# Performance work log

Measured on AMD Instinct MI355X. Metric: run time of the kernel, lower is better.

The kernel has to match this reference:

```python
import jax, jax.numpy as jnp
import numpy as np

LN_EPS = 1e-5


def setup_inputs() -> dict:
    key = jax.random.key(0)
    k1, k2, k3 = jax.random.split(key, 3)
    B, K, S, H, D = 8, 32, 4096, 2048, 1024
    plan_embeddings = jax.random.normal(k1, (B, S, H), dtype=jnp.float32)
    ownership = jax.random.bernoulli(k2, 0.5, (B, K, S))  # bool (B, K, S)
    W = jax.random.normal(k3, (H, D), dtype=jnp.float32) * (1.0 / np.sqrt(H))
    b = jnp.zeros((D,), dtype=jnp.float32)
    gamma = jnp.ones((D,), dtype=jnp.float32)
    beta = jnp.zeros((D,), dtype=jnp.float32)
    return {
        "plan_embeddings": plan_embeddings,
        "ownership": ownership,
        "W": W,
        "b": b,
        "gamma": gamma,
        "beta": beta,
    }


def reference(plan_embeddings, ownership, W, b, gamma, beta):
    # ownership-weighted mean pooling over slots S (same math as the
    # broadcast-multiply + sum in the torch original, expressed as an einsum
    # so no (B,K,S,H) intermediate is materialized)
    own_f = ownership.astype(plan_embeddings.dtype)          # (B, K, S)
    summed = jnp.einsum('bks,bsh->bkh', own_f, plan_embeddings)  # (B, K, H)
    counts = jnp.clip(own_f.sum(axis=-1, keepdims=True), 1.0)   # (B, K, 1)
    pooled = summed / counts                                   # (B, K, H)
    # linear projection
    projected = pooled @ W + b                                 # (B, K, D)
    # LayerNorm over last dim
    mu = projected.mean(axis=-1, keepdims=True)
    var = jnp.mean(jnp.square(projected - mu), axis=-1, keepdims=True)
    normed = (projected - mu) * jax.lax.rsqrt(var + LN_EPS)
    return normed * gamma + beta
```

## Files before the change

### kernel.cpp

```cpp
#include <hip/hip_runtime.h>

typedef unsigned int u32;
typedef unsigned short u16;
typedef __attribute__((ext_vector_type(8))) short short8;
typedef __attribute__((ext_vector_type(4))) float f32x4;
typedef __attribute__((ext_vector_type(16))) float f32x16;

#define BB 8
#define KK 32
#define SS 4096
#define HH 2048
#define DD 1024
#define NSC 16
#define SC_S 256
#define CH (BB * KK * HH)

#define OFF_W16  0ull
#define OFF_WB   (2ull << 20)
#define OFF_PART (6ull << 20)
#define OFF_PQ   (23ull << 20)
#define OFF_PROJ (24ull << 20)

__device__ __forceinline__ u16 f2bf(float x) {
  u32 u = __float_as_uint(x);
  return (u16)((u + 0x7fffu + ((u >> 16) & 1u)) >> 16);
}

__global__ __launch_bounds__(256) void k_prep(const void* __restrict__ own,
                                              u16* __restrict__ w16,
                                              const float* __restrict__ W,
                                              u16* __restrict__ WB) {
  __shared__ float lds[64][65];
  const int t = threadIdx.x;

  if (blockIdx.x < BB * KK) {
    const int bk = blockIdx.x;
    __shared__ int s_mode;
    __shared__ int s_wcnt[4];
    __shared__ float s_inv;

    if (t < 64) {
      u32 w = ((const u32*)own)[t];
      bool wordok = (w <= 1u) || (w == 0x3f800000u);
      unsigned long long m = __ballot(wordok);
      if (t == 0) s_mode = (m == ~0ull) ? 1 : 0;
    }
    __syncthreads();
    const int mode = s_mode;

    u32 bits = 0;
    const size_t base = (size_t)bk * SS + (size_t)t * 16;
    if (mode == 0) {
      uint4 v = *(const uint4*)((const unsigned char*)own + base);
      u32 wa[4] = {v.x, v.y, v.z, v.w};
#pragma unroll
      for (int w = 0; w < 4; ++w)
#pragma unroll
        for (int j = 0; j < 4; ++j)
          if ((wa[w] >> (8 * j)) & 0xffu) bits |= 1u << (4 * w + j);
    } else {
      const u32* p = (const u32*)own + base;
#pragma unroll
      for (int j = 0; j < 16; ++j)
        if (p[j] != 0u) bits |= 1u << j;
    }

    int cnt = __popc(bits);
#pragma unroll
    for (int off = 1; off < 64; off <<= 1) cnt += __shfl_xor(cnt, off);
    if ((t & 63) == 0) s_wcnt[t >> 6] = cnt;
    __syncthreads();
    if (t == 0) {
      int tot = s_wcnt[0] + s_wcnt[1] + s_wcnt[2] + s_wcnt[3];
      s_inv = 1.0f / fmaxf((float)tot, 1.0f);
    }
    __syncthreads();
    const u32 hv = (u32)f2bf(s_inv);

    u32 outw[8];
#pragma unroll
    for (int j = 0; j < 8; ++j) {
      u32 lo = ((bits >> (2 * j)) & 1u) ? hv : 0u;
      u32 hi = ((bits >> (2 * j + 1)) & 1u) ? hv : 0u;
      outw[j] = lo | (hi << 16);
    }
    u32* wo = (u32*)w16 + (size_t)bk * (SS / 2) + (size_t)t * 8;
    uint4 o0 = {outw[0], outw[1], outw[2], outw[3]};
    uint4 o1 = {outw[4], outw[5], outw[6], outw[7]};
    ((uint4*)wo)[0] = o0;
    ((uint4*)wo)[1] = o1;
  } else {
    const int bidx = blockIdx.x - BB * KK;
    const int hb = (bidx & 31) * 64, db = (bidx >> 5) * 64;
    const int x = t & 63, y = t >> 6;
#pragma unroll
    for (int j = 0; j < 16; ++j) {
      int r = y + 4 * j;
      lds[r][x] = W[(size_t)(hb + r) * DD + db + x];
    }
    __syncthreads();
#pragma unroll
    for (int j = 0; j < 16; ++j) {
      int r = y + 4 * j;
      WB[(size_t)(db + r) * HH + hb + x] = f2bf(lds[x][r]);
    }
  }
}

__global__ __launch_bounds__(1024, 4) void k_pool(const float* __restrict__ plan,
                                                  const u16* __restrict__ w16,
                                                  u16* __restrict__ part) {
  const int hcb = blockIdx.x, sc = blockIdx.y, b = blockIdx.z;
  const int t = threadIdx.x, wv = t >> 6, l = t & 63;
  const int lc = l & 31, half = l >> 5;
  const int h0 = hcb * 1024 + wv * 64;
  const int s0 = sc * SC_S;

  const float* pb = plan + (size_t)b * SS * HH + h0 + lc;
  const u16* wa = w16 + (size_t)(b * KK + lc) * SS;

  f32x16 acc0, acc1;
#pragma unroll
  for (int r = 0; r < 16; ++r) { acc0[r] = 0.0f; acc1[r] = 0.0f; }

  for (int step = 0; step < SC_S / 16; ++step) {
    const int sb = s0 + step * 16 + half * 8;
    short8 a = *(const short8*)(wa + sb);
    const float* col = pb + (size_t)sb * HH;
    float f0[8], f1[8];
#pragma unroll
    for (int j = 0; j < 8; ++j) {
      f0[j] = col[(size_t)j * HH];
      f1[j] = col[(size_t)j * HH + 32];
    }
    short8 b0, b1;
#pragma unroll
    for (int j = 0; j < 8; ++j) {
      b0[j] = (short)f2bf(f0[j]);
      b1[j] = (short)f2bf(f1[j]);
    }
    acc0 = __builtin_amdgcn_mfma_f32_32x32x16_bf16(a, b0, acc0, 0, 0, 0);
    acc1 = __builtin_amdgcn_mfma_f32_32x32x16_bf16(a, b1, acc1, 0, 0, 0);
  }

  u16* po = part + ((size_t)sc * BB + b) * KK * HH + h0 + lc;
#pragma unroll
  for (int r = 0; r < 16; ++r) {
    int krow = (r & 3) + 8 * (r >> 2) + 4 * half;
    po[(size_t)krow * HH] = f2bf(acc0[r]);
    po[(size_t)krow * HH + 32] = f2bf(acc1[r]);
  }
}

__global__ __launch_bounds__(256) void k_reduce(const u16* __restrict__ part,
                                                u32* __restrict__ pq) {
  const int i = blockIdx.x * 256 + threadIdx.x;
  const int row = i >> 10, hp = i & 1023;
  const u16* p = part + (size_t)row * HH + 2 * hp;
  float lo = 0.f, hi = 0.f;
#pragma unroll
  for (int sc = 0; sc < NSC; ++sc) {
    u32 v = *(const u32*)(p + (size_t)sc * CH);
    lo += __uint_as_float((v & 0xffffu) << 16);
    hi += __uint_as_float(v & 0xffff0000u);
  }
  pq[i] = (u32)f2bf(lo) | ((u32)f2bf(hi) << 16);
}

__global__ __launch_bounds__(256) void k_proj(const u16* __restrict__ pq,
                                              const u16* __restrict__ WB,
                                              const float* __restrict__ bias,
                                              float* __restrict__ proj) {
  const int rt = blockIdx.x, ctg = blockIdx.y;
  const int t = threadIdx.x, w = t >> 6, l = t & 63;
  const int lr = l & 15, lg = l >> 4;
  const int r0 = rt * 16, c0 = (ctg * 4 + w) * 16;

  const u16* pa = pq + (size_t)(r0 + lr) * HH + lg * 8;
  const u16* pw = WB + (size_t)(c0 + lr) * HH + lg * 8;
  f32x4 acc = (f32x4){0.f, 0.f, 0.f, 0.f};
#pragma unroll 4
  for (int slab = 0; slab < 64; ++slab) {
    short8 a = *(const short8*)(pa + slab * 32);
    short8 bv = *(const short8*)(pw + slab * 32);
    acc = __builtin_amdgcn_mfma_f32_16x16x32_bf16(a, bv, acc, 0, 0, 0);
  }
  const float bs = bias[c0 + lr];
#pragma unroll
  for (int j = 0; j < 4; ++j)
    proj[(size_t)(r0 + lg * 4 + j) * DD + c0 + lr] = acc[j] + bs;
}

__global__ __launch_bounds__(256) void k_ln(const float* __restrict__ proj,
                                            const float* __restrict__ gamma,
                                            const float* __restrict__ beta,
                                            float* __restrict__ out) {
  const int row = blockIdx.x, t = threadIdx.x;
  float4 v = ((const float4*)(proj + (size_t)row * DD))[t];
  float s1 = v.x + v.y + v.z + v.w;
  float s2 = v.x * v.x + v.y * v.y + v.z * v.z + v.w * v.w;
#pragma unroll
  for (int off = 1; off < 64; off <<= 1) {
    s1 += __shfl_xor(s1, off);
    s2 += __shfl_xor(s2, off);
  }
  __shared__ float a1[4], a2[4];
  if ((t & 63) == 0) { a1[t >> 6] = s1; a2[t >> 6] = s2; }
  __syncthreads();
  const float S1 = a1[0] + a1[1] + a1[2] + a1[3];
  const float S2 = a2[0] + a2[1] + a2[2] + a2[3];
  const float mu = S1 * (1.0f / DD);
  const float var = S2 * (1.0f / DD) - mu * mu;
  const float rs = rsqrtf(var + 1e-5f);
  float4 g = ((const float4*)gamma)[t];
  float4 be = ((const float4*)beta)[t];
  float4 o;
  o.x = (v.x - mu) * rs * g.x + be.x;
  o.y = (v.y - mu) * rs * g.y + be.y;
  o.z = (v.z - mu) * rs * g.z + be.z;
  o.w = (v.w - mu) * rs * g.w + be.w;
  ((float4*)(out + (size_t)row * DD))[t] = o;
}


extern "C" void kernel_launch(void* const* d_in, const int* in_sizes, int n_in,
                              void* d_out, int out_size, void* d_ws, size_t ws_size,
                              hipStream_t stream) {
  (void)in_sizes; (void)n_in; (void)out_size; (void)ws_size;
  const float* plan  = (const float*)d_in[0];
  const void*  own   = d_in[1];
  const float* W     = (const float*)d_in[2];
  const float* bias  = (const float*)d_in[3];
  const float* gamma = (const float*)d_in[4];
  const float* beta  = (const float*)d_in[5];
  float* out = (float*)d_out;
  char* ws = (char*)d_ws;

  u16*   w16  = (u16*)(ws + OFF_W16);
  u16*   WB   = (u16*)(ws + OFF_WB);
  u16*   part = (u16*)(ws + OFF_PART);
  u32*   pq   = (u32*)(ws + OFF_PQ);
  float* proj = (float*)(ws + OFF_PROJ);

  k_prep<<<dim3(BB * KK + (HH / 64) * (DD / 64)), dim3(256), 0, stream>>>(own, w16, W, WB);
  k_pool<<<dim3(2, NSC, BB), dim3(1024), 0, stream>>>(plan, w16, part);
  k_reduce<<<dim3((BB * KK * (HH / 2)) / 256), dim3(256), 0, stream>>>(part, pq);
  k_proj<<<dim3(16, 16), dim3(256), 0, stream>>>((const u16*)pq, WB, bias, proj);
  k_ln<<<dim3(BB * KK), dim3(256), 0, stream>>>(proj, gamma, beta, out);
}
```

Before: 84.02 us.

## Fuse all five stages into one cooperative persistent kernel with grid syncs

After: 212.8 us. 153% more time.

```diff
diff --git a/kernel.cpp b/kernel.cpp
--- a/kernel.cpp
+++ b/kernel.cpp
@@ -1,4 +1,7 @@
 #include <hip/hip_runtime.h>
+#include <hip/hip_cooperative_groups.h>
+
+namespace cg = cooperative_groups;
 
 typedef unsigned int u32;
 typedef unsigned short u16;
@@ -26,200 +29,207 @@
   return (u16)((u + 0x7fffu + ((u >> 16) & 1u)) >> 16);
 }
 
-__global__ __launch_bounds__(256) void k_prep(const void* __restrict__ own,
-                                              u16* __restrict__ w16,
-                                              const float* __restrict__ W,
-                                              u16* __restrict__ WB) {
-  __shared__ float lds[64][65];
+__global__ __launch_bounds__(1024, 4) void k_all(const float* __restrict__ plan,
+                                                 const void* __restrict__ own,
+                                                 const float* __restrict__ W,
+                                                 const float* __restrict__ bias,
+                                                 const float* __restrict__ gamma,
+                                                 const float* __restrict__ beta,
+                                                 float* __restrict__ out,
+                                                 u16* __restrict__ w16,
+                                                 u16* __restrict__ WB,
+                                                 u16* __restrict__ part,
+                                                 u32* __restrict__ pq,
+                                                 float* __restrict__ proj) {
+  cg::grid_group grid = cg::this_grid();
+  __shared__ float sP[4][16][64];
+  __shared__ float sLa[16], sLb[16];
+
+  const int blk = blockIdx.x;
   const int t = threadIdx.x;
-
-  if (blockIdx.x < BB * KK) {
-    const int bk = blockIdx.x;
-    __shared__ int s_mode;
-    __shared__ int s_wcnt[4];
-    __shared__ float s_inv;
-
-    if (t < 64) {
-      u32 w = ((const u32*)own)[t];
-      bool wordok = (w <= 1u) || (w == 0x3f800000u);
-      unsigned long long m = __ballot(wordok);
-      if (t == 0) s_mode = (m == ~0ull) ? 1 : 0;
-    }
-    __syncthreads();
-    const int mode = s_mode;
-
-    u32 bits = 0;
-    const size_t base = (size_t)bk * SS + (size_t)t * 16;
+  const int w = t >> 6, l = t & 63;
+
+  if (w == 0) {
+    u32 wd = ((const u32*)own)[l];
+    bool wordok = (wd <= 1u) || (wd == 0x3f800000u);
+    unsigned long long m = __ballot(wordok);
+    const int mode = (m == ~0ull) ? 1 : 0;
+
+    const size_t base = (size_t)blk * SS + (size_t)l * 64;
+    unsigned long long bits = 0;
     if (mode == 0) {
-      uint4 v = *(const uint4*)((const unsigned char*)own + base);
-      u32 wa[4] = {v.x, v.y, v.z, v.w};
-#pragma unroll
-      for (int w = 0; w < 4; ++w)
-#pragma unroll
-        for (int j = 0; j < 4; ++j)
-          if ((wa[w] >> (8 * j)) & 0xffu) bits |= 1u << (4 * w + j);
+      const uint4* p = (const uint4*)((const unsigned char*)own + base);
+#pragma unroll
+      for (int q = 0; q < 4; ++q) {
+        uint4 v = p[q];
+        u32 wa[4] = {v.x, v.y, v.z, v.w};
+#pragma unroll
+        for (int wj = 0; wj < 4; ++wj)
+#pragma unroll
+          for (int bj = 0; bj < 4; ++bj)
+            if ((wa[wj] >> (8 * bj)) & 0xffu)
+              bits |= 1ull << (q * 16 + wj * 4 + bj);
+      }
     } else {
       const u32* p = (const u32*)own + base;
 #pragma unroll
+      for (int j = 0; j < 64; ++j)
+        if (p[j] != 0u) bits |= 1ull << j;
+    }
+    int cnt = __popcll(bits);
+#pragma unroll
+    for (int off = 1; off < 64; off <<= 1) cnt += __shfl_xor(cnt, off);
+    const float inv = 1.0f / fmaxf((float)cnt, 1.0f);
+    const u32 hv = (u32)f2bf(inv);
+
+    u32* wo = (u32*)w16 + ((size_t)blk * SS + (size_t)l * 64) / 2;
+#pragma unroll
+    for (int q = 0; q < 8; ++q) {
+      u32 ww[4];
+#pragma unroll
+      for (int d = 0; d < 4; ++d) {
+        int j = q * 8 + d * 2;
+        u32 lo = ((bits >> j) & 1ull) ? hv : 0u;
+        u32 hi = ((bits >> (j + 1)) & 1ull) ? hv : 0u;
+        ww[d] = lo | (hi << 16);
+      }
+      uint4 o = {ww[0], ww[1], ww[2], ww[3]};
+      ((uint4*)wo)[q] = o;
+    }
+  } else {
+    int wt = blk * 15 + (w - 1);
+    if (wt < 2048) {
+      int hb = (wt >> 4) * 16;
+      int d0 = (wt & 15) * 64;
+      u16 rg[16];
+#pragma unroll
       for (int j = 0; j < 16; ++j)
-        if (p[j] != 0u) bits |= 1u << j;
-    }
-
-    int cnt = __popc(bits);
-#pragma unroll
-    for (int off = 1; off < 64; off <<= 1) cnt += __shfl_xor(cnt, off);
-    if ((t & 63) == 0) s_wcnt[t >> 6] = cnt;
+        rg[j] = f2bf(W[(size_t)(hb + j) * DD + d0 + l]);
+      u16* dst = WB + (size_t)(d0 + l) * HH + hb;
+#pragma unroll
+      for (int q = 0; q < 2; ++q) {
+        u32 ww[4];
+#pragma unroll
+        for (int d = 0; d < 4; ++d) {
+          int j = q * 8 + d * 2;
+          ww[d] = (u32)rg[j] | ((u32)rg[j + 1] << 16);
+        }
+        uint4 o = {ww[0], ww[1], ww[2], ww[3]};
+        ((uint4*)dst)[q] = o;
+      }
+    }
+  }
+
+  grid.sync();
+
+  {
+    const int hcb = blk & 1, sc = (blk >> 1) & 15, b = blk >> 5;
+    const int lc = l & 31, half = l >> 5;
+    const int h0 = hcb * 1024 + w * 64;
+    const int s0 = sc * SC_S;
+
+    const float* pb = plan + (size_t)b * SS * HH + h0 + lc;
+    const u16* wa = w16 + (size_t)(b * KK + lc) * SS;
+
+    f32x16 acc0, acc1;
+#pragma unroll
+    for (int r = 0; r < 16; ++r) { acc0[r] = 0.0f; acc1[r] = 0.0f; }
+
+    for (int step = 0; step < SC_S / 16; ++step) {
+      const int sb = s0 + step * 16 + half * 8;
+      short8 a = *(const short8*)(wa + sb);
+      const float* col = pb + (size_t)sb * HH;
+      float f0[8], f1[8];
+#pragma unroll
+      for (int j = 0; j < 8; ++j) {
+        f0[j] = col[(size_t)j * HH];
+        f1[j] = col[(size_t)j * HH + 32];
+      }
+      short8 b0, b1;
+#pragma unroll
+      for (int j = 0; j < 8; ++j) {
+        b0[j] = (short)f2bf(f0[j]);
+        b1[j] = (short)f2bf(f1[j]);
+      }
+      acc0 = __builtin_amdgcn_mfma_f32_32x32x16_bf16(a, b0, acc0, 0, 0, 0);
+      acc1 = __builtin_amdgcn_mfma_f32_32x32x16_bf16(a, b1, acc1, 0, 0, 0);
+    }
+
+    u16* po = part + ((size_t)sc * BB + b) * KK * HH + h0 + lc;
+#pragma unroll
+    for (int r = 0; r < 16; ++r) {
+      int krow = (r & 3) + 8 * (r >> 2) + 4 * half;
+      po[(size_t)krow * HH] = f2bf(acc0[r]);
+      po[(size_t)krow * HH + 32] = f2bf(acc1[r]);
+    }
+  }
+
+  grid.sync();
+
+  {
+    const int i = blk * 1024 + t;
+    const int row = i >> 10, hp = i & 1023;
+    const u16* p = part + (size_t)row * HH + 2 * hp;
+    float lo = 0.f, hi = 0.f;
+#pragma unroll
+    for (int sc = 0; sc < NSC; ++sc) {
+      u32 v = *(const u32*)(p + (size_t)sc * CH);
+      lo += __uint_as_float((v & 0xffffu) << 16);
+      hi += __uint_as_float(v & 0xffff0000u);
+    }
+    pq[i] = (u32)f2bf(lo) | ((u32)f2bf(hi) << 16);
+  }
+
+  grid.sync();
+
+  {
+    const int rt = blk >> 4, cq = blk & 15;
+    const int kq = w & 3, cw = w >> 2;
+    const int lr = l & 15, lg = l >> 4;
+    const int r0 = rt * 16, c0 = cq * 64;
+
+    const u16* pa = (const u16*)pq + (size_t)(r0 + lr) * HH + kq * 512 + lg * 8;
+    const u16* pw = WB + (size_t)(c0 + cw * 16 + lr) * HH + kq * 512 + lg * 8;
+    f32x4 acc = (f32x4){0.f, 0.f, 0.f, 0.f};
+#pragma unroll
+    for (int slab = 0; slab < 16; ++slab) {
+      short8 a = *(const short8*)(pa + slab * 32);
+      short8 bv = *(const short8*)(pw + slab * 32);
+      acc = __builtin_amdgcn_mfma_f32_16x16x32_bf16(a, bv, acc, 0, 0, 0);
+    }
+#pragma unroll
+    for (int j = 0; j < 4; ++j)
+      sP[kq][lg * 4 + j][cw * 16 + lr] = acc[j];
     __syncthreads();
-    if (t == 0) {
-      int tot = s_wcnt[0] + s_wcnt[1] + s_wcnt[2] + s_wcnt[3];
-      s_inv = 1.0f / fmaxf((float)tot, 1.0f);
-    }
+    {
+      int rr = t >> 6, cc = t & 63;
+      float v = sP[0][rr][cc] + sP[1][rr][cc] + sP[2][rr][cc] + sP[3][rr][cc]
+              + bias[c0 + cc];
+      proj[(size_t)(r0 + rr) * DD + c0 + cc] = v;
+    }
+  }
+
+  grid.sync();
+
+  {
+    const int row = blk;
+    float v = proj[(size_t)row * DD + t];
+    float s1 = v, s2 = v * v;
+#pragma unroll
+    for (int off = 1; off < 64; off <<= 1) {
+      s1 += __shfl_xor(s1, off);
+      s2 += __shfl_xor(s2, off);
+    }
+    if (l == 0) { sLa[w] = s1; sLb[w] = s2; }
     __syncthreads();
-    const u32 hv = (u32)f2bf(s_inv);
-
-    u32 outw[8];
-#pragma unroll
-    for (int j = 0; j < 8; ++j) {
-      u32 lo = ((bits >> (2 * j)) & 1u) ? hv : 0u;
-      u32 hi = ((bits >> (2 * j + 1)) & 1u) ? hv : 0u;
-      outw[j] = lo | (hi << 16);
-    }
-    u32* wo = (u32*)w16 + (size_t)bk * (SS / 2) + (size_t)t * 8;
-    uint4 o0 = {outw[0], outw[1], outw[2], outw[3]};
-    uint4 o1 = {outw[4], outw[5], outw[6], outw[7]};
-    ((uint4*)wo)[0] = o0;
-    ((uint4*)wo)[1] = o1;
-  } else {
-    const int bidx = blockIdx.x - BB * KK;
-    const int hb = (bidx & 31) * 64, db = (bidx >> 5) * 64;
-    const int x = t & 63, y = t >> 6;
-#pragma unroll
-    for (int j = 0; j < 16; ++j) {
-      int r = y + 4 * j;
-      lds[r][x] = W[(size_t)(hb + r) * DD + db + x];
-    }
-    __syncthreads();
-#pragma unroll
-    for (int j = 0; j < 16; ++j) {
-      int r = y + 4 * j;
-      WB[(size_t)(db + r) * HH + hb + x] = f2bf(lds[x][r]);
-    }
-  }
-}
-
-__global__ __launch_bounds__(1024, 4) void k_pool(const float* __restrict__ plan,
-                                                  const u16* __restrict__ w16,
-                                                  u16* __restrict__ part) {
-  const int hcb = blockIdx.x, sc = blockIdx.y, b = blockIdx.z;
-  const int t = threadIdx.x, wv = t >> 6, l = t & 63;
-  const int lc = l & 31, half = l >> 5;
-  const int h0 = hcb * 1024 + wv * 64;
-  const int s0 = sc * SC_S;
-
-  const float* pb = plan + (size_t)b * SS * HH + h0 + lc;
-  const u16* wa = w16 + (size_t)(b * KK + lc) * SS;
-
-  f32x16 acc0, acc1;
-#pragma unroll
-  for (int r = 0; r < 16; ++r) { acc0[r] = 0.0f; acc1[r] = 0.0f; }
-
-  for (int step = 0; step < SC_S / 16; ++step) {
-    const int sb = s0 + step * 16 + half * 8;
-    short8 a = *(const short8*)(wa + sb);
-    const float* col = pb + (size_t)sb * HH;
-    float f0[8], f1[8];
-#pragma unroll
-    for (int j = 0; j < 8; ++j) {
-      f0[j] = col[(size_t)j * HH];
-      f1[j] = col[(size_t)j * HH + 32];
-    }
-    short8 b0, b1;
-#pragma unroll
-    for (int j = 0; j < 8; ++j) {
-      b0[j] = (short)f2bf(f0[j]);
-      b1[j] = (short)f2bf(f1[j]);
-    }
-    acc0 = __builtin_amdgcn_mfma_f32_32x32x16_bf16(a, b0, acc0, 0, 0, 0);
-    acc1 = __builtin_amdgcn_mfma_f32_32x32x16_bf16(a, b1, acc1, 0, 0, 0);
-  }
-
-  u16* po = part + ((size_t)sc * BB + b) * KK * HH + h0 + lc;
-#pragma unroll
-  for (int r = 0; r < 16; ++r) {
-    int krow = (r & 3) + 8 * (r >> 2) + 4 * half;
-    po[(size_t)krow * HH] = f2bf(acc0[r]);
-    po[(size_t)krow * HH + 32] = f2bf(acc1[r]);
-  }
-}
-
-__global__ __launch_bounds__(256) void k_reduce(const u16* __restrict__ part,
-                                                u32* __restrict__ pq) {
-  const int i = blockIdx.x * 256 + threadIdx.x;
-  const int row = i >> 10, hp = i & 1023;
-  const u16* p = part + (size_t)row * HH + 2 * hp;
-  float lo = 0.f, hi = 0.f;
-#pragma unroll
-  for (int sc = 0; sc < NSC; ++sc) {
-    u32 v = *(const u32*)(p + (size_t)sc * CH);
-    lo += __uint_as_float((v & 0xffffu) << 16);
-    hi += __uint_as_float(v & 0xffff0000u);
-  }
-  pq[i] = (u32)f2bf(lo) | ((u32)f2bf(hi) << 16);
-}
-
-__global__ __launch_bounds__(256) void k_proj(const u16* __restrict__ pq,
-                                              const u16* __restrict__ WB,
-                                              const float* __restrict__ bias,
-                                              float* __restrict__ proj) {
-  const int rt = blockIdx.x, ctg = blockIdx.y;
-  const int t = threadIdx.x, w = t >> 6, l = t & 63;
-  const int lr = l & 15, lg = l >> 4;
-  const int r0 = rt * 16, c0 = (ctg * 4 + w) * 16;
-
-  const u16* pa = pq + (size_t)(r0 + lr) * HH + lg * 8;
-  const u16* pw = WB + (size_t)(c0 + lr) * HH + lg * 8;
-  f32x4 acc = (f32x4){0.f, 0.f, 0.f, 0.f};
-#pragma unroll 4
-  for (int slab = 0; slab < 64; ++slab) {
-    short8 a = *(const short8*)(pa + slab * 32);
-    short8 bv = *(const short8*)(pw + slab * 32);
-    acc = __builtin_amdgcn_mfma_f32_16x16x32_bf16(a, bv, acc, 0, 0, 0);
-  }
-  const float bs = bias[c0 + lr];
-#pragma unroll
-  for (int j = 0; j < 4; ++j)
-    proj[(size_t)(r0 + lg * 4 + j) * DD + c0 + lr] = acc[j] + bs;
-}
-
-__global__ __launch_bounds__(256) void k_ln(const float* __restrict__ proj,
-                                            const float* __restrict__ gamma,
-                                            const float* __restrict__ beta,
-                                            float* __restrict__ out) {
-  const int row = blockIdx.x, t = threadIdx.x;
-  float4 v = ((const float4*)(proj + (size_t)row * DD))[t];
-  float s1 = v.x + v.y + v.z + v.w;
-  float s2 = v.x * v.x + v.y * v.y + v.z * v.z + v.w * v.w;
-#pragma unroll
-  for (int off = 1; off < 64; off <<= 1) {
-    s1 += __shfl_xor(s1, off);
-    s2 += __shfl_xor(s2, off);
-  }
-  __shared__ float a1[4], a2[4];
-  if ((t & 63) == 0) { a1[t >> 6] = s1; a2[t >> 6] = s2; }
-  __syncthreads();
-  const float S1 = a1[0] + a1[1] + a1[2] + a1[3];
-  const float S2 = a2[0] + a2[1] + a2[2] + a2[3];
-  const float mu = S1 * (1.0f / DD);
-  const float var = S2 * (1.0f / DD) - mu * mu;
-  const float rs = rsqrtf(var + 1e-5f);
-  float4 g = ((const float4*)gamma)[t];
-  float4 be = ((const float4*)beta)[t];
-  float4 o;
-  o.x = (v.x - mu) * rs * g.x + be.x;
-  o.y = (v.y - mu) * rs * g.y + be.y;
-  o.z = (v.z - mu) * rs * g.z + be.z;
-  o.w = (v.w - mu) * rs * g.w + be.w;
-  ((float4*)(out + (size_t)row * DD))[t] = o;
+    float S1 = 0.f, S2 = 0.f;
+#pragma unroll
+    for (int q = 0; q < 16; ++q) { S1 += sLa[q]; S2 += sLb[q]; }
+    const float mu = S1 * (1.0f / DD);
+    const float var = S2 * (1.0f / DD) - mu * mu;
+    const float rs = rsqrtf(var + 1e-5f);
+    out[(size_t)row * DD + t] = (v - mu) * rs * gamma[t] + beta[t];
+  }
 }
 
 
@@ -242,9 +252,9 @@
   u32*   pq   = (u32*)(ws + OFF_PQ);
   float* proj = (float*)(ws + OFF_PROJ);
 
-  k_prep<<<dim3(BB * KK + (HH / 64) * (DD / 64)), dim3(256), 0, stream>>>(own, w16, W, WB);
-  k_pool<<<dim3(2, NSC, BB), dim3(1024), 0, stream>>>(plan, w16, part);
-  k_reduce<<<dim3((BB * KK * (HH / 2)) / 256), dim3(256), 0, stream>>>(part, pq);
-  k_proj<<<dim3(16, 16), dim3(256), 0, stream>>>((const u16*)pq, WB, bias, proj);
-  k_ln<<<dim3(BB * KK), dim3(256), 0, stream>>>(proj, gamma, beta, out);
+  void* args[] = {(void*)&plan, (void*)&own, (void*)&W, (void*)&bias,
+                  (void*)&gamma, (void*)&beta, (void*)&out, (void*)&w16,
+                  (void*)&WB, (void*)&part, (void*)&pq, (void*)&proj};
+  hipLaunchCooperativeKernel(reinterpret_cast<const void*>(k_all),
+                             dim3(256), dim3(1024), args, 0, stream);
 }
```

## Fuse ownership mask prep into pooling kernel and merge W transpose with reduce

Applied to the files above, without the earlier changes.

Result: slower. 95.39 us (+13.5%).

```diff
diff --git a/kernel.cpp b/kernel.cpp
--- a/kernel.cpp
+++ b/kernel.cpp
@@ -2,6 +2,8 @@
 
 typedef unsigned int u32;
 typedef unsigned short u16;
+typedef unsigned char u8;
+typedef unsigned long long u64;
 typedef __attribute__((ext_vector_type(8))) short short8;
 typedef __attribute__((ext_vector_type(4))) float f32x4;
 typedef __attribute__((ext_vector_type(16))) float f32x16;
@@ -15,7 +17,6 @@
 #define SC_S 256
 #define CH (BB * KK * HH)
 
-#define OFF_W16  0ull
 #define OFF_WB   (2ull << 20)
 #define OFF_PART (6ull << 20)
 #define OFF_PQ   (23ull << 20)
@@ -26,98 +27,58 @@
   return (u16)((u + 0x7fffu + ((u >> 16) & 1u)) >> 16);
 }
 
-__global__ __launch_bounds__(256) void k_prep(const void* __restrict__ own,
-                                              u16* __restrict__ w16,
-                                              const float* __restrict__ W,
-                                              u16* __restrict__ WB) {
-  __shared__ float lds[64][65];
-  const int t = threadIdx.x;
-
-  if (blockIdx.x < BB * KK) {
-    const int bk = blockIdx.x;
-    __shared__ int s_mode;
-    __shared__ int s_wcnt[4];
-    __shared__ float s_inv;
-
-    if (t < 64) {
-      u32 w = ((const u32*)own)[t];
-      bool wordok = (w <= 1u) || (w == 0x3f800000u);
-      unsigned long long m = __ballot(wordok);
-      if (t == 0) s_mode = (m == ~0ull) ? 1 : 0;
-    }
-    __syncthreads();
-    const int mode = s_mode;
-
-    u32 bits = 0;
-    const size_t base = (size_t)bk * SS + (size_t)t * 16;
-    if (mode == 0) {
-      uint4 v = *(const uint4*)((const unsigned char*)own + base);
-      u32 wa[4] = {v.x, v.y, v.z, v.w};
-#pragma unroll
-      for (int w = 0; w < 4; ++w)
-#pragma unroll
-        for (int j = 0; j < 4; ++j)
-          if ((wa[w] >> (8 * j)) & 0xffu) bits |= 1u << (4 * w + j);
-    } else {
-      const u32* p = (const u32*)own + base;
-#pragma unroll
-      for (int j = 0; j < 16; ++j)
-        if (p[j] != 0u) bits |= 1u << j;
-    }
-
-    int cnt = __popc(bits);
-#pragma unroll
-    for (int off = 1; off < 64; off <<= 1) cnt += __shfl_xor(cnt, off);
-    if ((t & 63) == 0) s_wcnt[t >> 6] = cnt;
-    __syncthreads();
-    if (t == 0) {
-      int tot = s_wcnt[0] + s_wcnt[1] + s_wcnt[2] + s_wcnt[3];
-      s_inv = 1.0f / fmaxf((float)tot, 1.0f);
-    }
-    __syncthreads();
-    const u32 hv = (u32)f2bf(s_inv);
-
-    u32 outw[8];
-#pragma unroll
-    for (int j = 0; j < 8; ++j) {
-      u32 lo = ((bits >> (2 * j)) & 1u) ? hv : 0u;
-      u32 hi = ((bits >> (2 * j + 1)) & 1u) ? hv : 0u;
-      outw[j] = lo | (hi << 16);
-    }
-    u32* wo = (u32*)w16 + (size_t)bk * (SS / 2) + (size_t)t * 8;
-    uint4 o0 = {outw[0], outw[1], outw[2], outw[3]};
-    uint4 o1 = {outw[4], outw[5], outw[6], outw[7]};
-    ((uint4*)wo)[0] = o0;
-    ((uint4*)wo)[1] = o1;
-  } else {
-    const int bidx = blockIdx.x - BB * KK;
-    const int hb = (bidx & 31) * 64, db = (bidx >> 5) * 64;
-    const int x = t & 63, y = t >> 6;
-#pragma unroll
-    for (int j = 0; j < 16; ++j) {
-      int r = y + 4 * j;
-      lds[r][x] = W[(size_t)(hb + r) * DD + db + x];
-    }
-    __syncthreads();
-#pragma unroll
-    for (int j = 0; j < 16; ++j) {
-      int r = y + 4 * j;
-      WB[(size_t)(db + r) * HH + hb + x] = f2bf(lds[x][r]);
-    }
-  }
+__device__ __forceinline__ int nzb(u32 x) {
+  return __popc((((x & 0x7F7F7F7Fu) + 0x7F7F7F7Fu) | x) & 0x80808080u);
 }
 
 __global__ __launch_bounds__(1024, 4) void k_pool(const float* __restrict__ plan,
-                                                  const u16* __restrict__ w16,
+                                                  const void* __restrict__ own,
                                                   u16* __restrict__ part) {
+  __shared__ float s_inv[KK];
+  __shared__ int s_mode;
   const int hcb = blockIdx.x, sc = blockIdx.y, b = blockIdx.z;
   const int t = threadIdx.x, wv = t >> 6, l = t & 63;
   const int lc = l & 31, half = l >> 5;
+
+  if (t < 64) {
+    u32 wd = ((const u32*)own)[t];
+    bool wordok = (wd <= 1u) || (wd == 0x3f800000u);
+    unsigned long long m = __ballot(wordok);
+    if (t == 0) s_mode = (m == ~0ull) ? 1 : 0;
+  }
+  __syncthreads();
+  const int mode = s_mode;
+
+  {
+    const int k = t >> 5, g = t & 31;
+    int cnt = 0;
+    if (mode == 0) {
+      const uint4* p = (const uint4*)((const u8*)own + (size_t)(b * KK + k) * SS);
+#pragma unroll
+      for (int i = 0; i < 8; ++i) {
+        uint4 v = p[g * 8 + i];
+        cnt += nzb(v.x) + nzb(v.y) + nzb(v.z) + nzb(v.w);
+      }
+    } else {
+      const uint4* p = (const uint4*)((const u32*)own + (size_t)(b * KK + k) * SS);
+#pragma unroll
+      for (int i = 0; i < 32; ++i) {
+        uint4 v = p[g * 32 + i];
+        cnt += (v.x != 0u) + (v.y != 0u) + (v.z != 0u) + (v.w != 0u);
+      }
+    }
+#pragma unroll
+    for (int off = 1; off < 32; off <<= 1) cnt += __shfl_xor(cnt, off);
+    if (g == 0) s_inv[k] = 1.0f / fmaxf((float)cnt, 1.0f);
+  }
+  __syncthreads();
+
   const int h0 = hcb * 1024 + wv * 64;
   const int s0 = sc * SC_S;
-
   const float* pb = plan + (size_t)b * SS * HH + h0 + lc;
-  const u16* wa = w16 + (size_t)(b * KK + lc) * SS;
+  const u16 hv = f2bf(s_inv[lc]);
+  const u8* obl = (const u8*)own + (size_t)(b * KK + lc) * SS;
+  const u32* owl = (const u32*)own + (size_t)(b * KK + lc) * SS;
 
   f32x16 acc0, acc1;
 #pragma unroll
@@ -125,7 +86,20 @@
 
   for (int step = 0; step < SC_S / 16; ++step) {
     const int sb = s0 + step * 16 + half * 8;
-    short8 a = *(const short8*)(wa + sb);
+    short8 a;
+    if (mode == 0) {
+      u64 msk = *(const u64*)(obl + sb);
+#pragma unroll
+      for (int j = 0; j < 8; ++j)
+        a[j] = (short)(((msk >> (8 * j)) & 0xffull) ? hv : (u16)0);
+    } else {
+      uint4 w0 = *(const uint4*)(owl + sb);
+      uint4 w1 = *(const uint4*)(owl + sb + 4);
+      u32 wa[8] = {w0.x, w0.y, w0.z, w0.w, w1.x, w1.y, w1.z, w1.w};
+#pragma unroll
+      for (int j = 0; j < 8; ++j)
+        a[j] = (short)(wa[j] ? hv : (u16)0);
+    }
     const float* col = pb + (size_t)sb * HH;
     float f0[8], f1[8];
 #pragma unroll
@@ -152,19 +126,41 @@
   }
 }
 
-__global__ __launch_bounds__(256) void k_reduce(const u16* __restrict__ part,
-                                                u32* __restrict__ pq) {
-  const int i = blockIdx.x * 256 + threadIdx.x;
-  const int row = i >> 10, hp = i & 1023;
-  const u16* p = part + (size_t)row * HH + 2 * hp;
-  float lo = 0.f, hi = 0.f;
-#pragma unroll
-  for (int sc = 0; sc < NSC; ++sc) {
-    u32 v = *(const u32*)(p + (size_t)sc * CH);
-    lo += __uint_as_float((v & 0xffffu) << 16);
-    hi += __uint_as_float(v & 0xffff0000u);
-  }
-  pq[i] = (u32)f2bf(lo) | ((u32)f2bf(hi) << 16);
+__global__ __launch_bounds__(256) void k_mid(const u16* __restrict__ part,
+                                             u32* __restrict__ pq,
+                                             const float* __restrict__ W,
+                                             u16* __restrict__ WB) {
+  __shared__ float lds[64][65];
+  const int t = threadIdx.x;
+
+  if (blockIdx.x < 1024) {
+    const int i = blockIdx.x * 256 + t;
+    const int row = i >> 10, hp = i & 1023;
+    const u16* p = part + (size_t)row * HH + 2 * hp;
+    float lo = 0.f, hi = 0.f;
+#pragma unroll
+    for (int sc = 0; sc < NSC; ++sc) {
+      u32 v = *(const u32*)(p + (size_t)sc * CH);
+      lo += __uint_as_float((v & 0xffffu) << 16);
+      hi += __uint_as_float(v & 0xffff0000u);
+    }
+    pq[i] = (u32)f2bf(lo) | ((u32)f2bf(hi) << 16);
+  } else {
+    const int bidx = blockIdx.x - 1024;
+    const int hb = (bidx & 31) * 64, db = (bidx >> 5) * 64;
+    const int x = t & 63, y = t >> 6;
+#pragma unroll
+    for (int j = 0; j < 16; ++j) {
+      int r = y + 4 * j;
+      lds[r][x] = W[(size_t)(hb + r) * DD + db + x];
+    }
+    __syncthreads();
+#pragma unroll
+    for (int j = 0; j < 16; ++j) {
+      int r = y + 4 * j;
+      WB[(size_t)(db + r) * HH + hb + x] = f2bf(lds[x][r]);
+    }
+  }
 }
 
 __global__ __launch_bounds__(256) void k_proj(const u16* __restrict__ pq,
@@ -236,15 +232,13 @@
   float* out = (float*)d_out;
   char* ws = (char*)d_ws;
 
-  u16*   w16  = (u16*)(ws + OFF_W16);
   u16*   WB   = (u16*)(ws + OFF_WB);
   u16*   part = (u16*)(ws + OFF_PART);
   u32*   pq   = (u32*)(ws + OFF_PQ);
   float* proj = (float*)(ws + OFF_PROJ);
 
-  k_prep<<<dim3(BB * KK + (HH / 64) * (DD / 64)), dim3(256), 0, stream>>>(own, w16, W, WB);
-  k_pool<<<dim3(2, NSC, BB), dim3(1024), 0, stream>>>(plan, w16, part);
-  k_reduce<<<dim3((BB * KK * (HH / 2)) / 256), dim3(256), 0, stream>>>(part, pq);
+  k_pool<<<dim3(2, NSC, BB), dim3(1024), 0, stream>>>(plan, own, part);
+  k_mid<<<dim3(1536), dim3(256), 0, stream>>>(part, pq, W, WB);
   k_proj<<<dim3(16, 16), dim3(256), 0, stream>>>((const u16*)pq, WB, bias, proj);
   k_ln<<<dim3(BB * KK), dim3(256), 0, stream>>>(proj, gamma, beta, out);
 }
```
